# Performance work log

Hardware: AMD Instinct MI355X
Metric: run time of the kernel (lower is better)

## Reference

```python
import jax, jax.numpy as jnp
import numpy as np

L = 8            # gat_blocks(4) * layers(2)
LAYERS = 2
RC, DC, SC, EC = 32, 32, 256, 512
IN_DIM, OUT_DIM = 2, 12
N_NODES, EMB, D_ATT = 512, 16, 16
B, T_IN = 8, 13  # T_IN == receptive_field -> no left padding


def setup_inputs() -> dict:
    key = jax.random.key(0)
    ks = jax.random.split(key, 12)
    g = lambda k, shp: jax.random.normal(k, shp, jnp.float32) * 0.05
    return {
        "input": jax.random.normal(ks[0], (B, IN_DIM, N_NODES, T_IN), jnp.float32),
        "gat_supports": jax.random.normal(ks[1], (EMB, N_NODES), jnp.float32),
        "start_w": g(ks[2], (RC, IN_DIM)), "start_b": jnp.zeros((RC,), jnp.float32),
        "filt_w": g(ks[3], (L, DC, RC, 1, 2)), "filt_b": jnp.zeros((L, DC), jnp.float32),
        "gate_w": g(ks[4], (L, DC, RC, 1, 2)), "gate_b": jnp.zeros((L, DC), jnp.float32),
        "skip_w": g(ks[5], (L, SC, DC)), "skip_b": jnp.zeros((L, SC), jnp.float32),
        "q_w": g(ks[6], (L, D_ATT, DC + EMB)), "q_b": jnp.zeros((L, D_ATT), jnp.float32),
        "k_w": g(ks[7], (L, D_ATT, DC + EMB)), "k_b": jnp.zeros((L, D_ATT), jnp.float32),
        "gmlp_w": g(ks[8], (L, RC, 2 * DC)), "gmlp_b": jnp.zeros((L, RC), jnp.float32),
        "bn_g": jnp.ones((L, RC), jnp.float32), "bn_b": jnp.zeros((L, RC), jnp.float32),
        "end1_w": g(ks[9], (EC, SC)), "end1_b": jnp.zeros((EC,), jnp.float32),
        "end2_w": g(ks[10], (OUT_DIM, EC)), "end2_b": jnp.zeros((OUT_DIM,), jnp.float32),
    }


def _pw(x, w, b):
    # 1x1 conv (pointwise linear over channels): x [B,C,N,T], w [O,C]
    return jnp.einsum('oc,bcnt->bont', w, x) + b[None, :, None, None]


def _tconv(x, w, b, d):
    # dilated temporal conv, kernel (1,2), VALID (shrinks T by d)
    y = jax.lax.conv_general_dilated(
        x, w, window_strides=(1, 1), padding='VALID', rhs_dilation=(1, d),
        dimension_numbers=('NCHW', 'OIHW', 'NCHW'))
    return y + b[None, :, None, None]


def _bn(x, g, b, eps=1e-5):
    # BatchNorm2d (training-mode batch stats, biased variance, as in torch)
    m = jnp.mean(x, axis=(0, 2, 3), keepdims=True)
    v = jnp.var(x, axis=(0, 2, 3), keepdims=True)
    return g[None, :, None, None] * (x - m) * jax.lax.rsqrt(v + eps) + b[None, :, None, None]


def _forward(input, gat_supports, start_w, start_b, filt_w, filt_b, gate_w, gate_b,
             skip_w, skip_b, q_w, q_b, k_w, k_b, gmlp_w, gmlp_b, bn_g, bn_b,
             end1_w, end1_b, end2_w, end2_b):
    x = _pw(input, start_w, start_b)          # [B,RC,N,T]
    skip = None
    scale = 1.0 / (D_ATT ** 0.5)
    for i in range(L):
        d = 2 ** (i % LAYERS)                 # dilation schedule 1,2 per block
        residual = x
        f = jnp.tanh(_tconv(residual, filt_w[i], filt_b[i], d))
        gt = jax.nn.sigmoid(_tconv(residual, gate_w[i], gate_b[i], d))
        x = f * gt                            # [B,DC,N,T-d]
        s = _pw(x, skip_w[i], skip_b[i])      # [B,SC,N,T-d]
        skip = s if skip is None else s + skip[:, :, :, -s.shape[3]:]
        # --- adaptive graph attention ---
        Bn, C, N, T = x.shape
        emb = jnp.broadcast_to(gat_supports[None, :, :, None], (Bn, EMB, N, T))
        xe = jnp.concatenate([x, emb], axis=1)            # [B,C+EMB,N,T]
        q = _pw(xe, q_w[i], q_b[i]).transpose(0, 3, 2, 1)  # [B,T,N,d]
        kk = _pw(xe, k_w[i], k_b[i]).transpose(0, 3, 2, 1)
        att = jax.nn.softmax(jnp.einsum('btnd,btmd->btnm', q, kk) * scale, axis=-1)
        xa = jnp.einsum('bcvt,btvw->bcwt', x, att)         # x @ att on node axis
        x = _pw(jnp.concatenate([x, xa], axis=1), gmlp_w[i], gmlp_b[i])
        # ---------------------------------
        x = x + residual[:, :, :, -x.shape[3]:]
        x = _bn(x, bn_g[i], bn_b[i])
    out = jax.nn.relu(skip)
    out = jax.nn.relu(_pw(out, end1_w, end1_b))
    out = _pw(out, end2_w, end2_b)            # [B,OUT_DIM,N,1]
    return out


def reference(input, gat_supports, start_w, start_b, filt_w, filt_b, gate_w, gate_b,
              skip_w, skip_b, q_w, q_b, k_w, k_b, gmlp_w, gmlp_b, bn_g, bn_b,
              end1_w, end1_b, end2_w, end2_b):
    return _forward(input, gat_supports, start_w, start_b, filt_w, filt_b, gate_w,
                    gate_b, skip_w, skip_b, q_w, q_b, k_w, k_b, gmlp_w, gmlp_b,
                    bn_g, bn_b, end1_w, end1_b, end2_w, end2_b)
```

## Files before the change

kernel.cpp:

```cpp
#include <hip/hip_runtime.h>
#include <math.h>


typedef short v4s __attribute__((ext_vector_type(4)));
typedef float v4f __attribute__((ext_vector_type(4)));
typedef unsigned short ushort_t;

#define MFMA16(a,b,c) __builtin_amdgcn_mfma_f32_16x16x16bf16_1k(a, b, c, 0, 0, 0)

__device__ inline ushort_t f2bf(float f){
    unsigned int u = __builtin_bit_cast(unsigned int, f);
    u += 0x7FFFu + ((u >> 16) & 1u);
    return (ushort_t)(u >> 16);
}
__device__ inline float bf2f(ushort_t h){
    return __builtin_bit_cast(float, ((unsigned int)h) << 16);
}

__global__ void k_emb(const float* __restrict__ qw, const float* __restrict__ qb,
                      const float* __restrict__ kw, const float* __restrict__ kb,
                      const float* __restrict__ gat, float* __restrict__ qe, float* __restrict__ ke){
    int idx = blockIdx.x*256 + threadIdx.x;
    const int total = 8*512*16;
    if (idx >= 2*total) return;
    bool isK = idx >= total;
    int id = isK ? idx - total : idx;
    int dq = id & 15; int n = (id >> 4) & 511; int l = id >> 13;
    const float* w = isK ? kw : qw;
    const float* bi = isK ? kb : qb;
    float acc = bi[l*16 + dq];
    const float* wrow = w + (l*16 + dq)*48 + 32;
    #pragma unroll
    for (int e = 0; e < 16; e++) acc += wrow[e] * gat[e*512 + n];
    (isK ? ke : qe)[(l*512 + n)*16 + dq] = isK ? acc : acc*0.25f;
}

__global__ void k_start(const float* __restrict__ inp, const float* __restrict__ sw,
                        const float* __restrict__ sb, float* __restrict__ x0){
    int idx = blockIdx.x*256 + threadIdx.x;
    if (idx >= 8*13*32*512) return;
    int n = idx & 511; int c = (idx >> 9) & 31; int r = idx >> 14;
    int t = r % 13; int b = r / 13;
    float v0 = inp[((b*2 + 0)*512 + n)*13 + t];
    float v1 = inp[((b*2 + 1)*512 + n)*13 + t];
    x0[idx] = sb[c] + sw[c*2 + 0]*v0 + sw[c*2 + 1]*v1;
}

__global__ void k_wprep(const float* __restrict__ filt_w, const float* __restrict__ gate_w,
                        const float* __restrict__ q_w, const float* __restrict__ k_w,
                        const float* __restrict__ skip_w,
                        const float* __restrict__ w1, const float* __restrict__ w2,
                        ushort_t* __restrict__ cwh, ushort_t* __restrict__ cwl,
                        ushort_t* __restrict__ qkw,
                        ushort_t* __restrict__ swh, ushort_t* __restrict__ swl,
                        ushort_t* __restrict__ w1h, ushort_t* __restrict__ w1l,
                        ushort_t* __restrict__ w2h, ushort_t* __restrict__ w2l)
{
    int idx = blockIdx.x*256 + threadIdx.x;
    if (idx < 32768){
        int k = idx & 63, o = (idx >> 6) & 63, l = idx >> 12;
        int c = k & 31, tap = k >> 5;
        float w = (o < 32) ? filt_w[((l*32 + o)*32 + c)*2 + tap]
                           : gate_w[((l*32 + (o-32))*32 + c)*2 + tap];
        ushort_t hi = f2bf(w);
        cwh[idx] = hi; cwl[idx] = f2bf(w - bf2f(hi));
    } else if (idx < 40960){
        int j2 = idx - 32768;
        int c = j2 & 31, j = (j2 >> 5) & 31, l = j2 >> 10;
        float w = (j < 16) ? q_w[(l*16 + j)*48 + c]*0.25f : k_w[(l*16 + (j-16))*48 + c];
        qkw[j2] = f2bf(w);
    } else if (idx < 106496){
        int s = idx - 40960;
        float w = skip_w[s];
        ushort_t hi = f2bf(w);
        swh[s] = hi; swl[s] = f2bf(w - bf2f(hi));
    } else if (idx < 237568){
        int s = idx - 106496;
        float w = w1[s];
        ushort_t hi = f2bf(w);
        w1h[s] = hi; w1l[s] = f2bf(w - bf2f(hi));
    } else if (idx < 245760){
        int s = idx - 237568;
        int od = s >> 9, k = s & 511;
        float w = (od < 12) ? w2[od*512 + k] : 0.0f;
        ushort_t hi = f2bf(w);
        w2h[s] = hi; w2l[s] = f2bf(w - bf2f(hi));
    }
}

__global__ __launch_bounds__(256) void k_gated_mfma(
    const float* __restrict__ xin, int Tin, int d, int Tout,
    const float* __restrict__ bnsumP, const float* __restrict__ bnG,
    const float* __restrict__ bnB, int ident, float cnt,
    const ushort_t* __restrict__ cwh, const ushort_t* __restrict__ cwl,
    const float* __restrict__ fb, const float* __restrict__ gb,
    const ushort_t* __restrict__ qkw,
    const float* __restrict__ qe, const float* __restrict__ ke,
    const ushort_t* __restrict__ swh, const ushort_t* __restrict__ swl,
    const float* __restrict__ sb,
    float* __restrict__ skip,
    ushort_t* __restrict__ xbfT, ushort_t* __restrict__ qbf, ushort_t* __restrict__ kbf,
    int do_qk)
{
    __shared__ unsigned int XBP[64*129];
    __shared__ float ABsh[64];
    int tid = threadIdx.x;
    int nch = blockIdx.x, t = blockIdx.y, b = blockIdx.z;
    size_t bt = (size_t)(b*Tout + t);
    int n0 = nch*128;
    int lane = tid & 63, wid = tid >> 6;
    int m16 = lane & 15, g4 = (lane >> 4)*4;

    if (tid < 32){
        float A, Bc;
        if (ident){ A = 1.0f; Bc = 0.0f; }
        else {
            float S = bnsumP[2*tid], S2 = bnsumP[2*tid + 1];
            float m = S/cnt, var = S2/cnt - m*m;
            A = bnG[tid]*rsqrtf(var + 1e-5f);
            Bc = bnB[tid] - m*A;
        }
        ABsh[tid] = A; ABsh[32 + tid] = Bc;
    }
    __syncthreads();

    #pragma unroll
    for (int kk = 0; kk < 16; kk++){
        int k = wid*16 + kk;
        int c = k & 31, tap = k >> 5;
        const float* src = xin + ((size_t)(b*Tin + t + tap*d)*32 + c)*512 + n0 + lane;
        float An = ABsh[c], Bn = ABsh[32 + c];
        #pragma unroll
        for (int h = 0; h < 2; h++){
            float xn = An*src[h*64] + Bn;
            ushort_t hi = f2bf(xn);
            ushort_t lo = f2bf(xn - bf2f(hi));
            XBP[k*129 + h*64 + lane] = (unsigned int)hi | ((unsigned int)lo << 16);
        }
    }
    v4s ah[4][4], al[4][4];
    #pragma unroll
    for (int ot = 0; ot < 4; ot++)
    #pragma unroll
    for (int kt = 0; kt < 4; kt++){
        ah[ot][kt] = *(const v4s*)(cwh + (ot*16 + m16)*64 + kt*16 + g4);
        al[ot][kt] = *(const v4s*)(cwl + (ot*16 + m16)*64 + kt*16 + g4);
    }
    v4f acc[4][2];
    #pragma unroll
    for (int ot = 0; ot < 4; ot++){
        float4 bv = *(const float4*)((ot < 2 ? fb + ot*16 : gb + (ot-2)*16) + g4);
        acc[ot][0] = (v4f){bv.x, bv.y, bv.z, bv.w};
        acc[ot][1] = (v4f){bv.x, bv.y, bv.z, bv.w};
    }
    __syncthreads();
    v4s bh[2][4], bl[2][4];
    #pragma unroll
    for (int nt = 0; nt < 2; nt++){
        int nl = (wid*2 + nt)*16 + m16;
        #pragma unroll
        for (int kt = 0; kt < 4; kt++){
            unsigned int u0 = XBP[(kt*16 + g4 + 0)*129 + nl];
            unsigned int u1 = XBP[(kt*16 + g4 + 1)*129 + nl];
            unsigned int u2 = XBP[(kt*16 + g4 + 2)*129 + nl];
            unsigned int u3 = XBP[(kt*16 + g4 + 3)*129 + nl];
            v4s hh, ll;
            hh[0] = (short)(u0 & 0xffffu); ll[0] = (short)(u0 >> 16);
            hh[1] = (short)(u1 & 0xffffu); ll[1] = (short)(u1 >> 16);
            hh[2] = (short)(u2 & 0xffffu); ll[2] = (short)(u2 >> 16);
            hh[3] = (short)(u3 & 0xffffu); ll[3] = (short)(u3 >> 16);
            bh[nt][kt] = hh; bl[nt][kt] = ll;
        }
    }
    #pragma unroll
    for (int kt = 0; kt < 4; kt++)
    #pragma unroll
    for (int ot = 0; ot < 4; ot++)
    #pragma unroll
    for (int nt = 0; nt < 2; nt++){
        acc[ot][nt] = MFMA16(ah[ot][kt], bh[nt][kt], acc[ot][nt]);
        acc[ot][nt] = MFMA16(ah[ot][kt], bl[nt][kt], acc[ot][nt]);
        acc[ot][nt] = MFMA16(al[ot][kt], bh[nt][kt], acc[ot][nt]);
    }
    v4s xh[2][2], xl[2][2];
    #pragma unroll
    for (int ct = 0; ct < 2; ct++)
    #pragma unroll
    for (int nt = 0; nt < 2; nt++){
        v4s hh, ll;
        #pragma unroll
        for (int i = 0; i < 4; i++){
            float f = acc[ct][nt][i], g = acc[ct+2][nt][i];
            float e2 = __expf(2.0f*f);
            float th = 1.0f - 2.0f/(e2 + 1.0f);
            float sg = 1.0f/(1.0f + __expf(-g));
            float v = th*sg;
            ushort_t hi = f2bf(v);
            hh[i] = (short)hi; ll[i] = (short)f2bf(v - bf2f(hi));
        }
        xh[ct][nt] = hh; xl[ct][nt] = ll;
    }
    if (do_qk){
        #pragma unroll
        for (int ct = 0; ct < 2; ct++)
        #pragma unroll
        for (int nt = 0; nt < 2; nt++){
            int nl = n0 + (wid*2 + nt)*16 + m16;
            #pragma unroll
            for (int i = 0; i < 4; i++)
                xbfT[(bt*32 + ct*16 + g4 + i)*512 + nl] = (ushort_t)xh[ct][nt][i];
        }
        v4s qa[2][2];
        #pragma unroll
        for (int ot = 0; ot < 2; ot++)
        #pragma unroll
        for (int kt = 0; kt < 2; kt++)
            qa[ot][kt] = *(const v4s*)(qkw + (ot*16 + m16)*32 + kt*16 + g4);
        #pragma unroll
        for (int ot = 0; ot < 2; ot++)
        #pragma unroll
        for (int nt = 0; nt < 2; nt++){
            int nl = n0 + (wid*2 + nt)*16 + m16;
            float4 ev = *(const float4*)((ot == 0 ? qe : ke) + nl*16 + g4);
            v4f a2 = (v4f){ev.x, ev.y, ev.z, ev.w};
            #pragma unroll
            for (int kt = 0; kt < 2; kt++)
                a2 = MFMA16(qa[ot][kt], xh[kt][nt], a2);
            v4s r;
            #pragma unroll
            for (int i = 0; i < 4; i++) r[i] = (short)f2bf(a2[i]);
            *(v4s*)((ot == 0 ? qbf : kbf) + (bt*512 + nl)*16 + g4) = r;
        }
    }
    if (t == Tout - 1){
        #pragma unroll 4
        for (int ot = 0; ot < 16; ot++){
            v4s sh_[2], sl_[2];
            #pragma unroll
            for (int kt = 0; kt < 2; kt++){
                sh_[kt] = *(const v4s*)(swh + (ot*16 + m16)*32 + kt*16 + g4);
                sl_[kt] = *(const v4s*)(swl + (ot*16 + m16)*32 + kt*16 + g4);
            }
            float4 sbv = *(const float4*)(sb + ot*16 + g4);
            #pragma unroll
            for (int nt = 0; nt < 2; nt++){
                int nl = n0 + (wid*2 + nt)*16 + m16;
                float* sp = skip + ((size_t)(b*512) + nl)*256 + ot*16 + g4;
                float4 old = *(const float4*)sp;
                v4f a3 = (v4f){old.x + sbv.x, old.y + sbv.y, old.z + sbv.z, old.w + sbv.w};
                #pragma unroll
                for (int kt = 0; kt < 2; kt++){
                    a3 = MFMA16(sh_[kt], xh[kt][nt], a3);
                    a3 = MFMA16(sh_[kt], xl[kt][nt], a3);
                    a3 = MFMA16(sl_[kt], xh[kt][nt], a3);
                }
                *(float4*)sp = make_float4(a3[0], a3[1], a3[2], a3[3]);
            }
        }
    }
}

__global__ __launch_bounds__(256) void k_z(
    const ushort_t* __restrict__ qbf, const ushort_t* __restrict__ kbf,
    int Tout, float* __restrict__ rz)
{
    __shared__ ushort_t KS[512*20];
    int tid = threadIdx.x;
    int vchunk = blockIdx.x, t = blockIdx.y, b = blockIdx.z;
    size_t bt = (size_t)(b*Tout + t);
    const ushort_t* kg = kbf + bt*8192;
    const ushort_t* qg = qbf + bt*8192;
    {
        const uint2* s0 = (const uint2*)(kg + tid*16);
        uint2* d0 = (uint2*)(KS + tid*20);
        d0[0]=s0[0]; d0[1]=s0[1]; d0[2]=s0[2]; d0[3]=s0[3];
        const uint2* s1 = (const uint2*)(kg + (tid+256)*16);
        uint2* d1 = (uint2*)(KS + (tid+256)*20);
        d1[0]=s1[0]; d1[1]=s1[1]; d1[2]=s1[2]; d1[3]=s1[3];
    }
    int l = tid & 63, wid = tid >> 6;
    int m16 = l & 15, g4 = (l >> 4)*4;
    __syncthreads();
    #pragma unroll
    for (int vi = 0; vi < 2; vi++){
        int vt = vchunk*8 + wid*2 + vi;
        v4s bq = *(const v4s*)(qg + (vt*16 + m16)*16 + g4);
        float zp = 0.f;
        for (int wt = 0; wt < 32; wt++){
            v4s ak = *(const v4s*)(KS + (wt*16 + m16)*20 + g4);
            v4f s = MFMA16(ak, bq, ((v4f){0.f,0.f,0.f,0.f}));
            zp += __expf(fminf(s[0],60.f)) + __expf(fminf(s[1],60.f))
                + __expf(fminf(s[2],60.f)) + __expf(fminf(s[3],60.f));
        }
        zp += __shfl_xor(zp, 16);
        zp += __shfl_xor(zp, 32);
        if (l < 16) rz[bt*512 + vt*16 + l] = 1.0f/zp;
    }
}

__global__ __launch_bounds__(256) void k_pv(
    const ushort_t* __restrict__ qbf, const ushort_t* __restrict__ kbf,
    const ushort_t* __restrict__ xbfT, const float* __restrict__ rz,
    const float* __restrict__ xin, int Tin, int d, int Tout,
    const float* __restrict__ bnsumP, const float* __restrict__ bnG,
    const float* __restrict__ bnB, int ident, float cnt,
    const float* __restrict__ gw, const float* __restrict__ gb,
    float* __restrict__ y, float* __restrict__ bnsumOut)
{
    __shared__ ushort_t QS[512*20];
    __shared__ ushort_t XT[32*520];
    __shared__ float rzs[512];
    __shared__ float bnsh[256];
    __shared__ float ABsh[64];
    int tid = threadIdx.x;
    int wc = blockIdx.x, t = blockIdx.y, b = blockIdx.z;
    size_t bt = (size_t)(b*Tout + t);
    const ushort_t* qg = qbf + bt*8192;
    const ushort_t* kg = kbf + bt*8192;
    {
        const uint2* s0 = (const uint2*)(qg + tid*16);
        uint2* d0 = (uint2*)(QS + tid*20);
        d0[0]=s0[0]; d0[1]=s0[1]; d0[2]=s0[2]; d0[3]=s0[3];
        const uint2* s1 = (const uint2*)(qg + (tid+256)*16);
        uint2* d1 = (uint2*)(QS + (tid+256)*20);
        d1[0]=s1[0]; d1[1]=s1[1]; d1[2]=s1[2]; d1[3]=s1[3];
        int c = tid >> 3, seg = tid & 7;
        const uint4* xs = (const uint4*)(xbfT + bt*16384 + c*512 + seg*64);
        uint4* xd = (uint4*)(XT + c*520 + seg*64);
        #pragma unroll
        for (int j = 0; j < 8; j++) xd[j] = xs[j];
        rzs[tid] = rz[bt*512 + tid];
        rzs[tid + 256] = rz[bt*512 + tid + 256];
    }
    if (tid < 32){
        float A, Bc;
        if (ident){ A = 1.0f; Bc = 0.0f; }
        else {
            float S = bnsumP[2*tid], S2 = bnsumP[2*tid + 1];
            float m = S/cnt, var = S2/cnt - m*m;
            A = bnG[tid]*rsqrtf(var + 1e-5f);
            Bc = bnB[tid] - m*A;
        }
        ABsh[tid] = A; ABsh[32 + tid] = Bc;
    }
    int l = tid & 63, wid = tid >> 6;
    int m16 = l & 15, g4 = (l >> 4)*4;
    v4s AG[2][2][2];
    #pragma unroll
    for (int pt = 0; pt < 2; pt++)
    #pragma unroll
    for (int ot = 0; ot < 2; ot++)
    #pragma unroll
    for (int ct = 0; ct < 2; ct++){
        float4 gv = *(const float4*)(gw + (ot*16 + m16)*64 + pt*32 + ct*16 + g4);
        v4s r; r[0] = (short)f2bf(gv.x); r[1] = (short)f2bf(gv.y);
        r[2] = (short)f2bf(gv.z); r[3] = (short)f2bf(gv.w);
        AG[pt][ot][ct] = r;
    }
    v4f gbv[2];
    #pragma unroll
    for (int ot = 0; ot < 2; ot++) gbv[ot] = *(const v4f*)(gb + ot*16 + g4);
    int wt0 = wc*8 + wid*2;
    v4s bk[2];
    bk[0] = *(const v4s*)(kg + (wt0*16 + m16)*16 + g4);
    bk[1] = *(const v4s*)(kg + ((wt0+1)*16 + m16)*16 + g4);
    __syncthreads();
    v4f An[2], Bn[2];
    #pragma unroll
    for (int ot = 0; ot < 2; ot++){
        #pragma unroll
        for (int i = 0; i < 4; i++){
            An[ot][i] = ABsh[ot*16 + g4 + i];
            Bn[ot][i] = ABsh[32 + ot*16 + g4 + i];
        }
    }
    v4f c2[2][2];
    #pragma unroll
    for (int i = 0; i < 2; i++){ c2[i][0] = (v4f){0.f,0.f,0.f,0.f}; c2[i][1] = (v4f){0.f,0.f,0.f,0.f}; }
    for (int vt = 0; vt < 32; vt++){
        v4s aq = *(const v4s*)(QS + (vt*16 + m16)*20 + g4);
        v4f s0 = MFMA16(aq, bk[0], ((v4f){0.f,0.f,0.f,0.f}));
        v4f s1 = MFMA16(aq, bk[1], ((v4f){0.f,0.f,0.f,0.f}));
        v4f rzv = *(const v4f*)(rzs + vt*16 + g4);
        v4s p0, p1;
        #pragma unroll
        for (int i = 0; i < 4; i++){
            p0[i] = (short)f2bf(__expf(fminf(s0[i],60.f)) * rzv[i]);
            p1[i] = (short)f2bf(__expf(fminf(s1[i],60.f)) * rzv[i]);
        }
        #pragma unroll
        for (int ct = 0; ct < 2; ct++){
            v4s ax = *(const v4s*)(XT + (ct*16 + m16)*520 + vt*16 + g4);
            c2[0][ct] = MFMA16(ax, p0, c2[0][ct]);
            c2[1][ct] = MFMA16(ax, p1, c2[1][ct]);
        }
    }
    float bs1[2][4], bs2[2][4];
    #pragma unroll
    for (int ot = 0; ot < 2; ot++)
    #pragma unroll
    for (int i = 0; i < 4; i++){ bs1[ot][i] = 0.f; bs2[ot][i] = 0.f; }
    #pragma unroll
    for (int wtl = 0; wtl < 2; wtl++){
        int wt = wt0 + wtl;
        v4s bxa[2], bx[2];
        #pragma unroll
        for (int ct = 0; ct < 2; ct++){
            v4s r;
            #pragma unroll
            for (int i = 0; i < 4; i++) r[i] = (short)f2bf(c2[wtl][ct][i]);
            bxa[ct] = r;
            v4s q;
            #pragma unroll
            for (int i = 0; i < 4; i++) q[i] = (short)XT[(ct*16 + g4 + i)*520 + wt*16 + m16];
            bx[ct] = q;
        }
        v4f c3[2];
        #pragma unroll
        for (int ot = 0; ot < 2; ot++){
            c3[ot] = gbv[ot];
            #pragma unroll
            for (int ct = 0; ct < 2; ct++){
                c3[ot] = MFMA16(AG[1][ot][ct], bxa[ct], c3[ot]);
                c3[ot] = MFMA16(AG[0][ot][ct], bx[ct],  c3[ot]);
            }
        }
        int wg = wt*16 + m16;
        const float* resbase = xin + ((size_t)(b*Tin + t + d)*32)*512 + wg;
        float* ybase = y + (bt*32)*512 + wg;
        #pragma unroll
        for (int ot = 0; ot < 2; ot++){
            #pragma unroll
            for (int i = 0; i < 4; i++){
                int outc = ot*16 + g4 + i;
                float yv = c3[ot][i] + An[ot][i]*resbase[(size_t)outc*512] + Bn[ot][i];
                ybase[(size_t)outc*512] = yv;
                bs1[ot][i] += yv; bs2[ot][i] += yv*yv;
            }
        }
    }
    #pragma unroll
    for (int off = 1; off <= 8; off <<= 1){
        #pragma unroll
        for (int ot = 0; ot < 2; ot++)
        #pragma unroll
        for (int i = 0; i < 4; i++){
            bs1[ot][i] += __shfl_xor(bs1[ot][i], off);
            bs2[ot][i] += __shfl_xor(bs2[ot][i], off);
        }
    }
    if (m16 == 0){
        #pragma unroll
        for (int ot = 0; ot < 2; ot++)
        #pragma unroll
        for (int i = 0; i < 4; i++){
            int c = ot*16 + g4 + i;
            bnsh[(wid*32 + c)*2 + 0] = bs1[ot][i];
            bnsh[(wid*32 + c)*2 + 1] = bs2[ot][i];
        }
    }
    __syncthreads();
    if (tid < 64){
        int c = tid & 31, p = tid >> 5;
        float s = 0.f;
        #pragma unroll
        for (int w = 0; w < 4; w++) s += bnsh[(w*32 + c)*2 + p];
        atomicAdd(&bnsumOut[c*2 + p], s);
    }
}

__global__ __launch_bounds__(256) void k_end_all(
    const float* __restrict__ skip,
    const ushort_t* __restrict__ w1hi, const ushort_t* __restrict__ w1lo,
    const float* __restrict__ b1,
    const ushort_t* __restrict__ w2hi, const ushort_t* __restrict__ w2lo,
    const float* __restrict__ b2, float* __restrict__ out)
{
    __shared__ ushort_t SH[16*264], SL[16*264];
    __shared__ ushort_t HH[512*17], HL[512*17];
    int tid = threadIdx.x;
    int nc = blockIdx.x, b = blockIdx.y;
    int n0 = nc*16;
    {
        int n = tid >> 4, s = tid & 15;
        const float4* src = (const float4*)(skip + ((size_t)(b*512 + n0 + n))*256 + s*16);
        #pragma unroll
        for (int j = 0; j < 4; j++){
            float4 v4_ = src[j];
            float vv[4] = {v4_.x, v4_.y, v4_.z, v4_.w};
            #pragma unroll
            for (int e = 0; e < 4; e++){
                float v = fmaxf(vv[e], 0.f);
                ushort_t h = f2bf(v);
                SH[n*264 + s*16 + j*4 + e] = h;
                SL[n*264 + s*16 + j*4 + e] = f2bf(v - bf2f(h));
            }
        }
    }
    __syncthreads();
    int l = tid & 63, wid = tid >> 6;
    int m16 = l & 15, g4 = (l >> 4)*4;
    v4f acc[8];
    #pragma unroll
    for (int nt = 0; nt < 8; nt++){
        float bo = b1[(wid*8 + nt)*16 + m16];
        acc[nt] = (v4f){bo, bo, bo, bo};
    }
    for (int kk = 0; kk < 16; kk++){
        v4s ahi = *(const v4s*)(SH + m16*264 + kk*16 + g4);
        v4s alo = *(const v4s*)(SL + m16*264 + kk*16 + g4);
        #pragma unroll
        for (int nt = 0; nt < 8; nt++){
            int o = (wid*8 + nt)*16 + m16;
            v4s bhi = *(const v4s*)(w1hi + o*256 + kk*16 + g4);
            v4s blo = *(const v4s*)(w1lo + o*256 + kk*16 + g4);
            acc[nt] = MFMA16(ahi, bhi, acc[nt]);
            acc[nt] = MFMA16(ahi, blo, acc[nt]);
            acc[nt] = MFMA16(alo, bhi, acc[nt]);
        }
    }
    #pragma unroll
    for (int nt = 0; nt < 8; nt++){
        int o = (wid*8 + nt)*16 + m16;
        #pragma unroll
        for (int i = 0; i < 4; i++){
            float v = fmaxf(acc[nt][i], 0.f);
            ushort_t h = f2bf(v);
            HH[o*17 + g4 + i] = h;
            HL[o*17 + g4 + i] = f2bf(v - bf2f(h));
        }
    }
    __syncthreads();
    if (wid == 0){
        v4f a4;
        #pragma unroll
        for (int i = 0; i < 4; i++){
            int od = g4 + i;
            a4[i] = (od < 12) ? b2[od] : 0.f;
        }
        for (int kt = 0; kt < 32; kt++){
            v4s wh, wl, hh, hl;
            #pragma unroll
            for (int i = 0; i < 4; i++){
                int k = kt*16 + g4 + i;
                wh[i] = (short)w2hi[m16*512 + k];
                wl[i] = (short)w2lo[m16*512 + k];
                hh[i] = (short)HH[k*17 + m16];
                hl[i] = (short)HL[k*17 + m16];
            }
            a4 = MFMA16(wh, hh, a4);
            a4 = MFMA16(wh, hl, a4);
            a4 = MFMA16(wl, hh, a4);
        }
        #pragma unroll
        for (int i = 0; i < 4; i++){
            int od = g4 + i;
            if (od < 12)
                out[((size_t)(b*12 + od))*512 + n0 + m16] = a4[i];
        }
    }
}

extern "C" void kernel_launch(void* const* d_in, const int* in_sizes, int n_in,
                              void* d_out, int out_size, void* d_ws, size_t ws_size,
                              hipStream_t stream)
{
    (void)in_sizes; (void)n_in; (void)out_size; (void)ws_size;
    const float* input  = (const float*)d_in[0];
    const float* gat    = (const float*)d_in[1];
    const float* start_w= (const float*)d_in[2];
    const float* start_b= (const float*)d_in[3];
    const float* filt_w = (const float*)d_in[4];
    const float* filt_b = (const float*)d_in[5];
    const float* gate_w = (const float*)d_in[6];
    const float* gate_b = (const float*)d_in[7];
    const float* skip_w = (const float*)d_in[8];
    const float* skip_b = (const float*)d_in[9];
    const float* q_w    = (const float*)d_in[10];
    const float* q_b    = (const float*)d_in[11];
    const float* k_w    = (const float*)d_in[12];
    const float* k_b    = (const float*)d_in[13];
    const float* gmlp_w = (const float*)d_in[14];
    const float* gmlp_b = (const float*)d_in[15];
    const float* bn_g   = (const float*)d_in[16];
    const float* bn_b   = (const float*)d_in[17];
    const float* end1_w = (const float*)d_in[18];
    const float* end1_b = (const float*)d_in[19];
    const float* end2_w = (const float*)d_in[20];
    const float* end2_b = (const float*)d_in[21];
    float* out = (float*)d_out;

    float* W = (float*)d_ws;
    size_t off = 0;
    float* skip = W + off; off += (size_t)8*512*256;
    float* bnsum= W + off; off += (size_t)7*64;
    float* bufA = W + off; off += (size_t)8*13*32*512;
    float* bufB = W + off; off += (size_t)8*13*32*512;
    float* qe   = W + off; off += (size_t)8*512*16;
    float* ke   = W + off; off += (size_t)8*512*16;
    float* rz   = W + off; off += (size_t)8*12*512;
    ushort_t* xbfT = (ushort_t*)(W + off); off += (size_t)8*12*32*512/2;
    ushort_t* qbf  = (ushort_t*)(W + off); off += (size_t)8*12*512*16/2;
    ushort_t* kbf  = (ushort_t*)(W + off); off += (size_t)8*12*512*16/2;
    ushort_t* cwh  = (ushort_t*)(W + off); off += (size_t)32768/2;
    ushort_t* cwl  = (ushort_t*)(W + off); off += (size_t)32768/2;
    ushort_t* qkw  = (ushort_t*)(W + off); off += (size_t)8192/2;
    ushort_t* swbh = (ushort_t*)(W + off); off += (size_t)65536/2;
    ushort_t* swbl = (ushort_t*)(W + off); off += (size_t)65536/2;
    ushort_t* w1hi = (ushort_t*)(W + off); off += (size_t)512*256/2;
    ushort_t* w1lo = (ushort_t*)(W + off); off += (size_t)512*256/2;
    ushort_t* w2hi = (ushort_t*)(W + off); off += (size_t)16*512/2;
    ushort_t* w2lo = (ushort_t*)(W + off); off += (size_t)16*512/2;

    hipMemsetAsync(skip, 0, ((size_t)8*512*256 + 7*64)*sizeof(float), stream);
    k_emb<<<512, 256, 0, stream>>>(q_w, q_b, k_w, k_b, gat, qe, ke);
    k_start<<<6656, 256, 0, stream>>>(input, start_w, start_b, bufA);
    k_wprep<<<960, 256, 0, stream>>>(filt_w, gate_w, q_w, k_w, skip_w, end1_w, end2_w,
                                     cwh, cwl, qkw, swbh, swbl, w1hi, w1lo, w2hi, w2lo);

    const int Tin[8] = {13,12,10,9,7,6,4,3};
    const int Dd[8]  = {1,2,1,2,1,2,1,2};
    float* xin = bufA; float* yb = bufB;
    for (int i = 0; i < 8; i++){
        int Ti = Tin[i], d = Dd[i], To = Ti - d;
        const float* bnsumP = (i == 0) ? bnsum : bnsum + (i-1)*64;
        const float* gP = (i == 0) ? bn_g : bn_g + (i-1)*32;
        const float* bP = (i == 0) ? bn_b : bn_b + (i-1)*32;
        int ident = (i == 0) ? 1 : 0;
        float cnt = 8.0f * (float)Ti * 512.0f;
        k_gated_mfma<<<dim3(4, To, 8), 256, 0, stream>>>(xin, Ti, d, To,
            bnsumP, gP, bP, ident, cnt,
            cwh + i*4096, cwl + i*4096, filt_b + i*32, gate_b + i*32,
            qkw + i*1024, qe + i*8192, ke + i*8192,
            swbh + i*8192, swbl + i*8192, skip_b + i*256,
            skip, xbfT, qbf, kbf, (i < 7) ? 1 : 0);
        if (i < 7){
            k_z<<<dim3(4, To, 8), 256, 0, stream>>>(qbf, kbf, To, rz);
            k_pv<<<dim3(4, To, 8), 256, 0, stream>>>(qbf, kbf, xbfT, rz,
                xin, Ti, d, To, bnsumP, gP, bP, ident, cnt,
                gmlp_w + i*2048, gmlp_b + i*32, yb, bnsum + i*64);
            float* tmp = xin; xin = yb; yb = tmp;
        }
    }
    k_end_all<<<dim3(32, 8), 256, 0, stream>>>(skip, w1hi, w1lo, end1_b, w2hi, w2lo, end2_b, out);
}
```

Before: 449.6 us.

## Merge prep kernels, double attention grid, repack end-MLP weights and split final GEMV

Fuses the memset, embedding, start-conv and weight-prep launches into a single k_prep kernel. Halves per-wave work in k_z and k_pv (one 16-wide tile per wave) and doubles their grid for more parallelism. Repacks end1/end2 weights into MFMA-tile-contiguous layout and spreads the final 512->12 projection across all four waves with an LDS reduction instead of wave 0 alone. Trade-offs: more blocks reload Q/K/X tiles into LDS, and the fused prep kernel has heavy branch divergence.

```diff
diff --git a/kernel.cpp b/kernel.cpp
--- a/kernel.cpp
+++ b/kernel.cpp
@@ -17,74 +17,82 @@
     return __builtin_bit_cast(float, ((unsigned int)h) << 16);
 }
 
-__global__ void k_emb(const float* __restrict__ qw, const float* __restrict__ qb,
-                      const float* __restrict__ kw, const float* __restrict__ kb,
-                      const float* __restrict__ gat, float* __restrict__ qe, float* __restrict__ ke){
+__global__ void k_prep(
+    const float* __restrict__ inp, const float* __restrict__ start_w, const float* __restrict__ start_b,
+    const float* __restrict__ gat,
+    const float* __restrict__ qw, const float* __restrict__ qb,
+    const float* __restrict__ kw, const float* __restrict__ kb,
+    const float* __restrict__ filt_w, const float* __restrict__ gate_w,
+    const float* __restrict__ skip_w,
+    const float* __restrict__ w1, const float* __restrict__ w2,
+    float* __restrict__ zero_base,
+    float* __restrict__ qe, float* __restrict__ ke, float* __restrict__ x0,
+    ushort_t* __restrict__ cwh, ushort_t* __restrict__ cwl, ushort_t* __restrict__ qkw,
+    ushort_t* __restrict__ swh, ushort_t* __restrict__ swl,
+    ushort_t* __restrict__ w1ph, ushort_t* __restrict__ w1pl,
+    ushort_t* __restrict__ w2ph, ushort_t* __restrict__ w2pl)
+{
+    const int E0 = 1049024;
+    const int E1 = E0 + 131072;
+    const int E2 = E1 + 1703936;
+    const int E3 = E2 + 32768;
+    const int E4 = E3 + 8192;
+    const int E5 = E4 + 65536;
+    const int E6 = E5 + 131072;
+    const int E7 = E6 + 8192;
     int idx = blockIdx.x*256 + threadIdx.x;
-    const int total = 8*512*16;
-    if (idx >= 2*total) return;
-    bool isK = idx >= total;
-    int id = isK ? idx - total : idx;
-    int dq = id & 15; int n = (id >> 4) & 511; int l = id >> 13;
-    const float* w = isK ? kw : qw;
-    const float* bi = isK ? kb : qb;
-    float acc = bi[l*16 + dq];
-    const float* wrow = w + (l*16 + dq)*48 + 32;
-    #pragma unroll
-    for (int e = 0; e < 16; e++) acc += wrow[e] * gat[e*512 + n];
-    (isK ? ke : qe)[(l*512 + n)*16 + dq] = isK ? acc : acc*0.25f;
-}
-
-__global__ void k_start(const float* __restrict__ inp, const float* __restrict__ sw,
-                        const float* __restrict__ sb, float* __restrict__ x0){
-    int idx = blockIdx.x*256 + threadIdx.x;
-    if (idx >= 8*13*32*512) return;
-    int n = idx & 511; int c = (idx >> 9) & 31; int r = idx >> 14;
-    int t = r % 13; int b = r / 13;
-    float v0 = inp[((b*2 + 0)*512 + n)*13 + t];
-    float v1 = inp[((b*2 + 1)*512 + n)*13 + t];
-    x0[idx] = sb[c] + sw[c*2 + 0]*v0 + sw[c*2 + 1]*v1;
-}
-
-__global__ void k_wprep(const float* __restrict__ filt_w, const float* __restrict__ gate_w,
-                        const float* __restrict__ q_w, const float* __restrict__ k_w,
-                        const float* __restrict__ skip_w,
-                        const float* __restrict__ w1, const float* __restrict__ w2,
-                        ushort_t* __restrict__ cwh, ushort_t* __restrict__ cwl,
-                        ushort_t* __restrict__ qkw,
-                        ushort_t* __restrict__ swh, ushort_t* __restrict__ swl,
-                        ushort_t* __restrict__ w1h, ushort_t* __restrict__ w1l,
-                        ushort_t* __restrict__ w2h, ushort_t* __restrict__ w2l)
-{
-    int idx = blockIdx.x*256 + threadIdx.x;
-    if (idx < 32768){
-        int k = idx & 63, o = (idx >> 6) & 63, l = idx >> 12;
+    if (idx < E0){
+        zero_base[idx] = 0.0f;
+    } else if (idx < E1){
+        int id = idx - E0;
+        const int total = 8*512*16;
+        bool isK = id >= total;
+        if (isK) id -= total;
+        int dq = id & 15; int n = (id >> 4) & 511; int l = id >> 13;
+        const float* w = isK ? kw : qw;
+        const float* bi = isK ? kb : qb;
+        float acc = bi[l*16 + dq];
+        const float* wrow = w + (l*16 + dq)*48 + 32;
+        #pragma unroll
+        for (int e = 0; e < 16; e++) acc += wrow[e] * gat[e*512 + n];
+        (isK ? ke : qe)[(l*512 + n)*16 + dq] = isK ? acc : acc*0.25f;
+    } else if (idx < E2){
+        int id = idx - E1;
+        int n = id & 511; int c = (id >> 9) & 31; int r = id >> 14;
+        int t = r % 13; int b = r / 13;
+        float v0 = inp[((b*2 + 0)*512 + n)*13 + t];
+        float v1 = inp[((b*2 + 1)*512 + n)*13 + t];
+        x0[id] = start_b[c] + start_w[c*2 + 0]*v0 + start_w[c*2 + 1]*v1;
+    } else if (idx < E3){
+        int id = idx - E2;
+        int k = id & 63, o = (id >> 6) & 63, l = id >> 12;
         int c = k & 31, tap = k >> 5;
         float w = (o < 32) ? filt_w[((l*32 + o)*32 + c)*2 + tap]
                            : gate_w[((l*32 + (o-32))*32 + c)*2 + tap];
         ushort_t hi = f2bf(w);
-        cwh[idx] = hi; cwl[idx] = f2bf(w - bf2f(hi));
-    } else if (idx < 40960){
-        int j2 = idx - 32768;
-        int c = j2 & 31, j = (j2 >> 5) & 31, l = j2 >> 10;
-        float w = (j < 16) ? q_w[(l*16 + j)*48 + c]*0.25f : k_w[(l*16 + (j-16))*48 + c];
-        qkw[j2] = f2bf(w);
-    } else if (idx < 106496){
-        int s = idx - 40960;
-        float w = skip_w[s];
+        cwh[id] = hi; cwl[id] = f2bf(w - bf2f(hi));
+    } else if (idx < E4){
+        int id = idx - E3;
+        int c = id & 31, j = (id >> 5) & 31, l = id >> 10;
+        float w = (j < 16) ? qw[(l*16 + j)*48 + c]*0.25f : kw[(l*16 + (j-16))*48 + c];
+        qkw[id] = f2bf(w);
+    } else if (idx < E5){
+        int id = idx - E4;
+        float w = skip_w[id];
         ushort_t hi = f2bf(w);
-        swh[s] = hi; swl[s] = f2bf(w - bf2f(hi));
-    } else if (idx < 237568){
-        int s = idx - 106496;
-        float w = w1[s];
+        swh[id] = hi; swl[id] = f2bf(w - bf2f(hi));
+    } else if (idx < E6){
+        int id = idx - E5;
+        int j = id & 15, m16 = (id >> 4) & 15, kk = (id >> 8) & 15, ot = id >> 12;
+        float w = w1[((size_t)(ot*16 + m16))*256 + kk*16 + j];
         ushort_t hi = f2bf(w);
-        w1h[s] = hi; w1l[s] = f2bf(w - bf2f(hi));
-    } else if (idx < 245760){
-        int s = idx - 237568;
-        int od = s >> 9, k = s & 511;
-        float w = (od < 12) ? w2[od*512 + k] : 0.0f;
+        w1ph[id] = hi; w1pl[id] = f2bf(w - bf2f(hi));
+    } else if (idx < E7){
+        int id = idx - E6;
+        int j = id & 15, m16 = (id >> 4) & 15, kt = id >> 8;
+        float w = (m16 < 12) ? w2[m16*512 + kt*16 + j] : 0.0f;
         ushort_t hi = f2bf(w);
-        w2h[s] = hi; w2l[s] = f2bf(w - bf2f(hi));
+        w2ph[id] = hi; w2pl[id] = f2bf(w - bf2f(hi));
     }
 }
 
@@ -281,21 +289,18 @@
     int l = tid & 63, wid = tid >> 6;
     int m16 = l & 15, g4 = (l >> 4)*4;
     __syncthreads();
-    #pragma unroll
-    for (int vi = 0; vi < 2; vi++){
-        int vt = vchunk*8 + wid*2 + vi;
-        v4s bq = *(const v4s*)(qg + (vt*16 + m16)*16 + g4);
-        float zp = 0.f;
-        for (int wt = 0; wt < 32; wt++){
-            v4s ak = *(const v4s*)(KS + (wt*16 + m16)*20 + g4);
-            v4f s = MFMA16(ak, bq, ((v4f){0.f,0.f,0.f,0.f}));
-            zp += __expf(fminf(s[0],60.f)) + __expf(fminf(s[1],60.f))
-                + __expf(fminf(s[2],60.f)) + __expf(fminf(s[3],60.f));
-        }
-        zp += __shfl_xor(zp, 16);
-        zp += __shfl_xor(zp, 32);
-        if (l < 16) rz[bt*512 + vt*16 + l] = 1.0f/zp;
-    }
+    int vt = vchunk*4 + wid;
+    v4s bq = *(const v4s*)(qg + (vt*16 + m16)*16 + g4);
+    float zp = 0.f;
+    for (int wt = 0; wt < 32; wt++){
+        v4s ak = *(const v4s*)(KS + (wt*16 + m16)*20 + g4);
+        v4f s = MFMA16(ak, bq, ((v4f){0.f,0.f,0.f,0.f}));
+        zp += __expf(fminf(s[0],60.f)) + __expf(fminf(s[1],60.f))
+            + __expf(fminf(s[2],60.f)) + __expf(fminf(s[3],60.f));
+    }
+    zp += __shfl_xor(zp, 16);
+    zp += __shfl_xor(zp, 32);
+    if (l < 16) rz[bt*512 + vt*16 + l] = 1.0f/zp;
 }
 
 __global__ __launch_bounds__(256) void k_pv(
@@ -360,10 +365,8 @@
     v4f gbv[2];
     #pragma unroll
     for (int ot = 0; ot < 2; ot++) gbv[ot] = *(const v4f*)(gb + ot*16 + g4);
-    int wt0 = wc*8 + wid*2;
-    v4s bk[2];
-    bk[0] = *(const v4s*)(kg + (wt0*16 + m16)*16 + g4);
-    bk[1] = *(const v4s*)(kg + ((wt0+1)*16 + m16)*16 + g4);
+    int wt = wc*4 + wid;
+    v4s bk = *(const v4s*)(kg + (wt*16 + m16)*16 + g4);
     __syncthreads();
     v4f An[2], Bn[2];
     #pragma unroll
@@ -374,25 +377,20 @@
             Bn[ot][i] = ABsh[32 + ot*16 + g4 + i];
         }
     }
-    v4f c2[2][2];
-    #pragma unroll
-    for (int i = 0; i < 2; i++){ c2[i][0] = (v4f){0.f,0.f,0.f,0.f}; c2[i][1] = (v4f){0.f,0.f,0.f,0.f}; }
+    v4f c2[2];
+    c2[0] = (v4f){0.f,0.f,0.f,0.f}; c2[1] = (v4f){0.f,0.f,0.f,0.f};
     for (int vt = 0; vt < 32; vt++){
         v4s aq = *(const v4s*)(QS + (vt*16 + m16)*20 + g4);
-        v4f s0 = MFMA16(aq, bk[0], ((v4f){0.f,0.f,0.f,0.f}));
-        v4f s1 = MFMA16(aq, bk[1], ((v4f){0.f,0.f,0.f,0.f}));
+        v4f s0 = MFMA16(aq, bk, ((v4f){0.f,0.f,0.f,0.f}));
         v4f rzv = *(const v4f*)(rzs + vt*16 + g4);
-        v4s p0, p1;
-        #pragma unroll
-        for (int i = 0; i < 4; i++){
+        v4s p0;
+        #pragma unroll
+        for (int i = 0; i < 4; i++)
             p0[i] = (short)f2bf(__expf(fminf(s0[i],60.f)) * rzv[i]);
-            p1[i] = (short)f2bf(__expf(fminf(s1[i],60.f)) * rzv[i]);
-        }
         #pragma unroll
         for (int ct = 0; ct < 2; ct++){
             v4s ax = *(const v4s*)(XT + (ct*16 + m16)*520 + vt*16 + g4);
-            c2[0][ct] = MFMA16(ax, p0, c2[0][ct]);
-            c2[1][ct] = MFMA16(ax, p1, c2[1][ct]);
+            c2[ct] = MFMA16(ax, p0, c2[ct]);
         }
     }
     float bs1[2][4], bs2[2][4];
@@ -400,15 +398,13 @@
     for (int ot = 0; ot < 2; ot++)
     #pragma unroll
     for (int i = 0; i < 4; i++){ bs1[ot][i] = 0.f; bs2[ot][i] = 0.f; }
-    #pragma unroll
-    for (int wtl = 0; wtl < 2; wtl++){
-        int wt = wt0 + wtl;
+    {
         v4s bxa[2], bx[2];
         #pragma unroll
         for (int ct = 0; ct < 2; ct++){
             v4s r;
             #pragma unroll
-            for (int i = 0; i < 4; i++) r[i] = (short)f2bf(c2[wtl][ct][i]);
+            for (int i = 0; i < 4; i++) r[i] = (short)f2bf(c2[ct][i]);
             bxa[ct] = r;
             v4s q;
             #pragma unroll
@@ -471,13 +467,14 @@
 
 __global__ __launch_bounds__(256) void k_end_all(
     const float* __restrict__ skip,
-    const ushort_t* __restrict__ w1hi, const ushort_t* __restrict__ w1lo,
+    const ushort_t* __restrict__ w1ph, const ushort_t* __restrict__ w1pl,
     const float* __restrict__ b1,
-    const ushort_t* __restrict__ w2hi, const ushort_t* __restrict__ w2lo,
+    const ushort_t* __restrict__ w2ph, const ushort_t* __restrict__ w2pl,
     const float* __restrict__ b2, float* __restrict__ out)
 {
     __shared__ ushort_t SH[16*264], SL[16*264];
-    __shared__ ushort_t HH[512*17], HL[512*17];
+    __shared__ ushort_t HH[512*18], HL[512*18];
+    __shared__ float PS[4][16][17];
     int tid = threadIdx.x;
     int nc = blockIdx.x, b = blockIdx.y;
     int n0 = nc*16;
@@ -511,9 +508,9 @@
         v4s alo = *(const v4s*)(SL + m16*264 + kk*16 + g4);
         #pragma unroll
         for (int nt = 0; nt < 8; nt++){
-            int o = (wid*8 + nt)*16 + m16;
-            v4s bhi = *(const v4s*)(w1hi + o*256 + kk*16 + g4);
-            v4s blo = *(const v4s*)(w1lo + o*256 + kk*16 + g4);
+            int ob = ((wid*8 + nt)*16 + kk)*256;
+            v4s bhi = *(const v4s*)(w1ph + ob + m16*16 + g4);
+            v4s blo = *(const v4s*)(w1pl + ob + m16*16 + g4);
             acc[nt] = MFMA16(ahi, bhi, acc[nt]);
             acc[nt] = MFMA16(ahi, blo, acc[nt]);
             acc[nt] = MFMA16(alo, bhi, acc[nt]);
@@ -526,37 +523,39 @@
         for (int i = 0; i < 4; i++){
             float v = fmaxf(acc[nt][i], 0.f);
             ushort_t h = f2bf(v);
-            HH[o*17 + g4 + i] = h;
-            HL[o*17 + g4 + i] = f2bf(v - bf2f(h));
-        }
-    }
+            HH[o*18 + g4 + i] = h;
+            HL[o*18 + g4 + i] = f2bf(v - bf2f(h));
+        }
+    }
+    __syncthreads();
+    v4f a4 = (v4f){0.f, 0.f, 0.f, 0.f};
+    for (int q = 0; q < 8; q++){
+        int kt = wid*8 + q;
+        v4s wh = *(const v4s*)(w2ph + kt*256 + m16*16 + g4);
+        v4s wl = *(const v4s*)(w2pl + kt*256 + m16*16 + g4);
+        v4s hh, hl;
+        #pragma unroll
+        for (int i = 0; i < 4; i++){
+            int k = kt*16 + g4 + i;
+            hh[i] = (short)HH[k*18 + m16];
+            hl[i] = (short)HL[k*18 + m16];
+        }
+        a4 = MFMA16(wh, hh, a4);
+        a4 = MFMA16(wh, hl, a4);
+        a4 = MFMA16(wl, hh, a4);
+    }
+    #pragma unroll
+    for (int i = 0; i < 4; i++) PS[wid][g4 + i][m16] = a4[i];
     __syncthreads();
     if (wid == 0){
-        v4f a4;
         #pragma unroll
         for (int i = 0; i < 4; i++){
             int od = g4 + i;
-            a4[i] = (od < 12) ? b2[od] : 0.f;
-        }
-        for (int kt = 0; kt < 32; kt++){
-            v4s wh, wl, hh, hl;
-            #pragma unroll
-            for (int i = 0; i < 4; i++){
-                int k = kt*16 + g4 + i;
-                wh[i] = (short)w2hi[m16*512 + k];
-                wl[i] = (short)w2lo[m16*512 + k];
-                hh[i] = (short)HH[k*17 + m16];
-                hl[i] = (short)HL[k*17 + m16];
+            if (od < 12){
+                float v = b2[od] + PS[0][od][m16] + PS[1][od][m16]
+                        + PS[2][od][m16] + PS[3][od][m16];
+                out[((size_t)(b*12 + od))*512 + n0 + m16] = v;
             }
-            a4 = MFMA16(wh, hh, a4);
-            a4 = MFMA16(wh, hl, a4);
-            a4 = MFMA16(wl, hh, a4);
-        }
-        #pragma unroll
-        for (int i = 0; i < 4; i++){
-            int od = g4 + i;
-            if (od < 12)
-                out[((size_t)(b*12 + od))*512 + n0 + m16] = a4[i];
         }
     }
 }
@@ -607,16 +606,15 @@
     ushort_t* qkw  = (ushort_t*)(W + off); off += (size_t)8192/2;
     ushort_t* swbh = (ushort_t*)(W + off); off += (size_t)65536/2;
     ushort_t* swbl = (ushort_t*)(W + off); off += (size_t)65536/2;
-    ushort_t* w1hi = (ushort_t*)(W + off); off += (size_t)512*256/2;
-    ushort_t* w1lo = (ushort_t*)(W + off); off += (size_t)512*256/2;
-    ushort_t* w2hi = (ushort_t*)(W + off); off += (size_t)16*512/2;
-    ushort_t* w2lo = (ushort_t*)(W + off); off += (size_t)16*512/2;
-
-    hipMemsetAsync(skip, 0, ((size_t)8*512*256 + 7*64)*sizeof(float), stream);
-    k_emb<<<512, 256, 0, stream>>>(q_w, q_b, k_w, k_b, gat, qe, ke);
-    k_start<<<6656, 256, 0, stream>>>(input, start_w, start_b, bufA);
-    k_wprep<<<960, 256, 0, stream>>>(filt_w, gate_w, q_w, k_w, skip_w, end1_w, end2_w,
-                                     cwh, cwl, qkw, swbh, swbl, w1hi, w1lo, w2hi, w2lo);
+    ushort_t* w1ph = (ushort_t*)(W + off); off += (size_t)512*256/2;
+    ushort_t* w1pl = (ushort_t*)(W + off); off += (size_t)512*256/2;
+    ushort_t* w2ph = (ushort_t*)(W + off); off += (size_t)16*512/2;
+    ushort_t* w2pl = (ushort_t*)(W + off); off += (size_t)16*512/2;
+
+    k_prep<<<12226, 256, 0, stream>>>(input, start_w, start_b, gat,
+        q_w, q_b, k_w, k_b, filt_w, gate_w, skip_w, end1_w, end2_w,
+        skip, qe, ke, bufA,
+        cwh, cwl, qkw, swbh, swbl, w1ph, w1pl, w2ph, w2pl);
 
     const int Tin[8] = {13,12,10,9,7,6,4,3};
     const int Dd[8]  = {1,2,1,2,1,2,1,2};
@@ -635,12 +633,12 @@
             swbh + i*8192, swbl + i*8192, skip_b + i*256,
             skip, xbfT, qbf, kbf, (i < 7) ? 1 : 0);
         if (i < 7){
-            k_z<<<dim3(4, To, 8), 256, 0, stream>>>(qbf, kbf, To, rz);
-            k_pv<<<dim3(4, To, 8), 256, 0, stream>>>(qbf, kbf, xbfT, rz,
+            k_z<<<dim3(8, To, 8), 256, 0, stream>>>(qbf, kbf, To, rz);
+            k_pv<<<dim3(8, To, 8), 256, 0, stream>>>(qbf, kbf, xbfT, rz,
                 xin, Ti, d, To, bnsumP, gP, bP, ident, cnt,
                 gmlp_w + i*2048, gmlp_b + i*32, yb, bnsum + i*64);
             float* tmp = xin; xin = yb; yb = tmp;
         }
     }
-    k_end_all<<<dim3(32, 8), 256, 0, stream>>>(skip, w1hi, w1lo, end1_b, w2hi, w2lo, end2_b, out);
-}
+    k_end_all<<<dim3(32, 8), 256, 0, stream>>>(skip, w1ph, w1pl, end1_b, w2ph, w2pl, end2_b, out);
+}
```

New measurement: 443.8 us. Within noise of the previous version (-1.3%).
